# Performance work log

Hardware: AMD Instinct MI355X
Metric: run time of the kernel (lower is better)

Reference implementation:

```python
import jax, jax.numpy as jnp
import numpy as np

TEMPERATURE = 0.5
EPS_NORM = 1e-12   # F.normalize eps
EPS_DEN = 1e-8     # denominator clamp


def setup_inputs() -> dict:
    key = jax.random.key(0)
    k1, k2 = jax.random.split(key)
    B, D = 4096, 256
    return {
        "proj_feat1": jax.random.normal(k1, (B, D), dtype=jnp.float32),
        "proj_feat2": jax.random.normal(k2, (B, D), dtype=jnp.float32),
    }


def _l2_normalize(x):
    n = jnp.sqrt(jnp.sum(x * x, axis=1, keepdims=True))
    return x / jnp.maximum(n, EPS_NORM)


def reference(proj_feat1, proj_feat2):
    B = proj_feat1.shape[0]
    z1 = _l2_normalize(proj_feat1)
    z2 = _l2_normalize(proj_feat2)
    z = jnp.concatenate([z1, z2], axis=0)          # [2B, D], unit rows
    # cosine similarity of unit-norm rows == plain matmul (GEMM instead of
    # the O(N^2*D) broadcasted intermediate in the torch source)
    sim = jnp.matmul(z, z.T)                        # [2B, 2B]
    s = jnp.exp(sim / TEMPERATURE)                  # [2B, 2B]
    idx = jnp.arange(2 * B)
    pos_idx = (idx + B) % (2 * B)                   # roll(eye, B, dim=1) positions
    numerator = s[idx, pos_idx]                     # [2B]
    # negatives: everything except the diagonal
    diag = jnp.diagonal(s)
    denominator = jnp.sum(s, axis=1) - diag         # sum * (1 - eye)
    denominator = jnp.maximum(denominator, EPS_DEN)
    loss = jnp.mean(-jnp.log(numerator / denominator))
    return loss
```

## Files before the change

### kernel.cpp

```cpp
#include <hip/hip_runtime.h>
#include <hip/hip_bf16.h>

#define NTOT 8192
#define BB   4096
#define DD   256

typedef __attribute__((ext_vector_type(8))) short short8v;
typedef __attribute__((ext_vector_type(4))) float f32x4;

__device__ __forceinline__ unsigned short f2bf(float f) {
    union { __hip_bfloat16 h; unsigned short u; } cv;
    cv.h = __float2bfloat16(f);
    return cv.u;
}

__global__ __launch_bounds__(256) void k_normalize(
    const float* __restrict__ x1, const float* __restrict__ x2,
    unsigned short* __restrict__ zbf,
    float* __restrict__ selfdot, float* __restrict__ posdot,
    float* __restrict__ out)
{
    if (blockIdx.x == 0 && threadIdx.x == 0) out[0] = 0.0f;

    const int lane = threadIdx.x & 63;
    const int pair = blockIdx.x * 4 + (threadIdx.x >> 6);

    const float4 a = *(const float4*)(x1 + (size_t)pair * DD + lane * 4);
    const float4 b = *(const float4*)(x2 + (size_t)pair * DD + lane * 4);

    float s1 = a.x * a.x + a.y * a.y + a.z * a.z + a.w * a.w;
    float s2 = b.x * b.x + b.y * b.y + b.z * b.z + b.w * b.w;
#pragma unroll
    for (int off = 1; off < 64; off <<= 1) {
        s1 += __shfl_xor(s1, off);
        s2 += __shfl_xor(s2, off);
    }
    const float inv1 = 1.0f / fmaxf(sqrtf(s1), 1e-12f);
    const float inv2 = 1.0f / fmaxf(sqrtf(s2), 1e-12f);

    const float4 z1 = make_float4(a.x * inv1, a.y * inv1, a.z * inv1, a.w * inv1);
    const float4 z2 = make_float4(b.x * inv2, b.y * inv2, b.z * inv2, b.w * inv2);

    float sd1 = z1.x * z1.x + z1.y * z1.y + z1.z * z1.z + z1.w * z1.w;
    float sd2 = z2.x * z2.x + z2.y * z2.y + z2.z * z2.z + z2.w * z2.w;
    float pd  = z1.x * z2.x + z1.y * z2.y + z1.z * z2.z + z1.w * z2.w;
#pragma unroll
    for (int off = 1; off < 64; off <<= 1) {
        sd1 += __shfl_xor(sd1, off);
        sd2 += __shfl_xor(sd2, off);
        pd  += __shfl_xor(pd, off);
    }

    ushort4 u1, u2;
    u1.x = f2bf(z1.x); u1.y = f2bf(z1.y); u1.z = f2bf(z1.z); u1.w = f2bf(z1.w);
    u2.x = f2bf(z2.x); u2.y = f2bf(z2.y); u2.z = f2bf(z2.z); u2.w = f2bf(z2.w);
    *(ushort4*)(zbf + (size_t)pair * DD + lane * 4) = u1;
    *(ushort4*)(zbf + (size_t)(pair + BB) * DD + lane * 4) = u2;

    if (lane == 0) {
        selfdot[pair] = sd1;
        selfdot[pair + BB] = sd2;
        posdot[pair] = pd;
        posdot[pair + BB] = pd;
    }
}

__global__ __launch_bounds__(256, 2) void k_simsum(
    const unsigned short* __restrict__ zbf, float* __restrict__ S_part)
{
    __shared__ char Bsh[2][32768];

    const int tid  = threadIdx.x;
    const int lane = tid & 63;
    const int wave = tid >> 6;
    const int frow = lane & 15;
    const int row0 = blockIdx.x * 256 + wave * 64;
    const int colStart = blockIdx.y * 512;

    short8v Afrag[4][8];
#pragma unroll
    for (int rt = 0; rt < 4; ++rt) {
        const int row = row0 + rt * 16 + frow;
        const unsigned short* ap = zbf + (size_t)row * DD + (lane >> 4) * 8;
#pragma unroll
        for (int kk = 0; kk < 8; ++kk)
            Afrag[rt][kk] = *(const short8v*)(ap + kk * 32);
    }
#pragma unroll
    for (int rt = 0; rt < 4; ++rt)
#pragma unroll
        for (int kk = 0; kk < 8; ++kk)
            asm volatile("" : "+v"(Afrag[rt][kk]));

    const int jswz = (tid & 31) ^ ((tid >> 5) & 7);
    const char* gsrc0 = (const char*)zbf + (size_t)colStart * 512
                        + (tid >> 5) * 512 + jswz * 16;

    const int base0 = frow * 512 + (lane >> 4) * 16;
    const int bmask = (frow & 7) << 4;

    float rs[4][4];
#pragma unroll
    for (int rt = 0; rt < 4; ++rt)
#pragma unroll
        for (int q = 0; q < 4; ++q) rs[rt][q] = 0.0f;

#pragma unroll
    for (int r = 0; r < 8; ++r)
        __builtin_amdgcn_global_load_lds(
            (const __attribute__((address_space(1))) unsigned int*)(gsrc0 + r * 4096),
            (__attribute__((address_space(3))) unsigned int*)(&Bsh[0][0] + tid * 16 + r * 4096),
            16, 0, 0);
    __syncthreads();

    int cur = 0;
    for (int t = 0; t < 8; ++t) {
        if (t < 7) {
            const char* gs = gsrc0 + (size_t)(t + 1) * 32768;
            char* ld = &Bsh[cur ^ 1][0] + tid * 16;
#pragma unroll
            for (int r = 0; r < 8; ++r)
                __builtin_amdgcn_global_load_lds(
                    (const __attribute__((address_space(1))) unsigned int*)(gs + r * 4096),
                    (__attribute__((address_space(3))) unsigned int*)(ld + r * 4096),
                    16, 0, 0);
        }

#pragma unroll
        for (int c2 = 0; c2 < 2; ++c2) {
            f32x4 acc[4][2];
#pragma unroll
            for (int rt = 0; rt < 4; ++rt)
#pragma unroll
                for (int c = 0; c < 2; ++c) {
                    acc[rt][c][0] = 0.0f; acc[rt][c][1] = 0.0f;
                    acc[rt][c][2] = 0.0f; acc[rt][c][3] = 0.0f;
                }

#pragma unroll
            for (int kk = 0; kk < 8; ++kk) {
                const char* bp = &Bsh[cur][0] + ((base0 + kk * 64) ^ bmask)
                                 + c2 * 16384;
                short8v b0 = *(const short8v*)(bp);
                short8v b1 = *(const short8v*)(bp + 8192);
#pragma unroll
                for (int rt = 0; rt < 4; ++rt) {
                    acc[rt][0] = __builtin_amdgcn_mfma_f32_16x16x32_bf16(
                        Afrag[rt][kk], b0, acc[rt][0], 0, 0, 0);
                    acc[rt][1] = __builtin_amdgcn_mfma_f32_16x16x32_bf16(
                        Afrag[rt][kk], b1, acc[rt][1], 0, 0, 0);
                }
            }

#pragma unroll
            for (int rt = 0; rt < 4; ++rt)
#pragma unroll
                for (int q = 0; q < 4; ++q)
                    rs[rt][q] += exp2f(acc[rt][0][q] * 2.8853900817779268f)
                               + exp2f(acc[rt][1][q] * 2.8853900817779268f);
        }

        __syncthreads();
        cur ^= 1;
    }

#pragma unroll
    for (int rt = 0; rt < 4; ++rt) {
#pragma unroll
        for (int q = 0; q < 4; ++q) {
            float v = rs[rt][q];
            v += __shfl_xor(v, 1);
            v += __shfl_xor(v, 2);
            v += __shfl_xor(v, 4);
            v += __shfl_xor(v, 8);
            if (frow == 0) {
                const int row = row0 + rt * 16 + (lane >> 4) * 4 + q;
                S_part[blockIdx.y * NTOT + row] = v;
            }
        }
    }
}

__global__ __launch_bounds__(256) void k_final(
    const float* __restrict__ S_part, const float* __restrict__ selfdot,
    const float* __restrict__ posdot, float* __restrict__ out)
{
    __shared__ float red[4];
    const int tid = threadIdx.x;
    const int i = blockIdx.x * 256 + tid;
    float s = 0.0f;
#pragma unroll
    for (int sp = 0; sp < 16; ++sp) s += S_part[sp * NTOT + i];
    const float den = fmaxf(s - expf(2.0f * selfdot[i]), 1e-8f);
    float acc = logf(den) - 2.0f * posdot[i];
#pragma unroll
    for (int off = 1; off < 64; off <<= 1) acc += __shfl_xor(acc, off);
    if ((tid & 63) == 0) red[tid >> 6] = acc;
    __syncthreads();
    if (tid == 0)
        atomicAdd(out, (red[0] + red[1] + red[2] + red[3]) * (1.0f / (float)NTOT));
}

extern "C" void kernel_launch(void* const* d_in, const int* in_sizes, int n_in,
                              void* d_out, int out_size, void* d_ws, size_t ws_size,
                              hipStream_t stream) {
    const float* x1 = (const float*)d_in[0];
    const float* x2 = (const float*)d_in[1];
    float* out = (float*)d_out;

    char* ws = (char*)d_ws;
    unsigned short* zbf = (unsigned short*)ws;
    size_t off = (size_t)NTOT * DD * sizeof(unsigned short);
    float* S_part = (float*)(ws + off);
    off += (size_t)16 * NTOT * sizeof(float);
    float* selfdot = (float*)(ws + off);
    off += (size_t)NTOT * sizeof(float);
    float* posdot = (float*)(ws + off);

    k_normalize<<<dim3(BB / 4), dim3(256), 0, stream>>>(x1, x2, zbf, selfdot, posdot, out);
    k_simsum<<<dim3(32, 16), dim3(256), 0, stream>>>(zbf, S_part);
    k_final<<<dim3(32), dim3(256), 0, stream>>>(S_part, selfdot, posdot, out);
}
```

Baseline: 108.2 us.

## Load B fragments directly from global memory, drop LDS double buffering

Replaces the LDS double-buffered staging of B tiles (global_load_lds, swizzling, barriers) with direct per-lane global loads of B fragments in 32-column chunks. Each wave now loads the same B data independently, relying on L1/L2 caching instead of shared memory. This removes barriers and LDS traffic, but it adds redundant global/L1 loads and exposes load latency to the MFMA loop. Grid sizes are now expressed through an NSTRIPE macro.

```diff
diff --git a/kernel.cpp b/kernel.cpp
--- a/kernel.cpp
+++ b/kernel.cpp
@@ -4,6 +4,7 @@
 #define NTOT 8192
 #define BB   4096
 #define DD   256
+#define NSTRIPE 16
 
 typedef __attribute__((ext_vector_type(8))) short short8v;
 typedef __attribute__((ext_vector_type(4))) float f32x4;
@@ -68,36 +69,22 @@
 __global__ __launch_bounds__(256, 2) void k_simsum(
     const unsigned short* __restrict__ zbf, float* __restrict__ S_part)
 {
-    __shared__ char Bsh[2][32768];
-
     const int tid  = threadIdx.x;
     const int lane = tid & 63;
     const int wave = tid >> 6;
     const int frow = lane & 15;
+    const int khalf = (lane >> 4) * 8;
     const int row0 = blockIdx.x * 256 + wave * 64;
     const int colStart = blockIdx.y * 512;
 
     short8v Afrag[4][8];
 #pragma unroll
     for (int rt = 0; rt < 4; ++rt) {
-        const int row = row0 + rt * 16 + frow;
-        const unsigned short* ap = zbf + (size_t)row * DD + (lane >> 4) * 8;
+        const unsigned short* ap = zbf + (size_t)(row0 + rt * 16 + frow) * DD + khalf;
 #pragma unroll
         for (int kk = 0; kk < 8; ++kk)
             Afrag[rt][kk] = *(const short8v*)(ap + kk * 32);
     }
-#pragma unroll
-    for (int rt = 0; rt < 4; ++rt)
-#pragma unroll
-        for (int kk = 0; kk < 8; ++kk)
-            asm volatile("" : "+v"(Afrag[rt][kk]));
-
-    const int jswz = (tid & 31) ^ ((tid >> 5) & 7);
-    const char* gsrc0 = (const char*)zbf + (size_t)colStart * 512
-                        + (tid >> 5) * 512 + jswz * 16;
-
-    const int base0 = frow * 512 + (lane >> 4) * 16;
-    const int bmask = (frow & 7) << 4;
 
     float rs[4][4];
 #pragma unroll
@@ -105,63 +92,39 @@
 #pragma unroll
         for (int q = 0; q < 4; ++q) rs[rt][q] = 0.0f;
 
+#pragma unroll 2
+    for (int ch = 0; ch < 16; ++ch) {
+        const unsigned short* bp = zbf
+            + (size_t)(colStart + ch * 32 + frow) * DD + khalf;
+
+        f32x4 acc[4][2];
 #pragma unroll
-    for (int r = 0; r < 8; ++r)
-        __builtin_amdgcn_global_load_lds(
-            (const __attribute__((address_space(1))) unsigned int*)(gsrc0 + r * 4096),
-            (__attribute__((address_space(3))) unsigned int*)(&Bsh[0][0] + tid * 16 + r * 4096),
-            16, 0, 0);
-    __syncthreads();
+        for (int rt = 0; rt < 4; ++rt)
+#pragma unroll
+            for (int c = 0; c < 2; ++c) {
+                acc[rt][c][0] = 0.0f; acc[rt][c][1] = 0.0f;
+                acc[rt][c][2] = 0.0f; acc[rt][c][3] = 0.0f;
+            }
 
-    int cur = 0;
-    for (int t = 0; t < 8; ++t) {
-        if (t < 7) {
-            const char* gs = gsrc0 + (size_t)(t + 1) * 32768;
-            char* ld = &Bsh[cur ^ 1][0] + tid * 16;
 #pragma unroll
-            for (int r = 0; r < 8; ++r)
-                __builtin_amdgcn_global_load_lds(
-                    (const __attribute__((address_space(1))) unsigned int*)(gs + r * 4096),
-                    (__attribute__((address_space(3))) unsigned int*)(ld + r * 4096),
-                    16, 0, 0);
+        for (int kk = 0; kk < 8; ++kk) {
+            const short8v b0 = *(const short8v*)(bp + kk * 32);
+            const short8v b1 = *(const short8v*)(bp + 16 * DD + kk * 32);
+#pragma unroll
+            for (int rt = 0; rt < 4; ++rt) {
+                acc[rt][0] = __builtin_amdgcn_mfma_f32_16x16x32_bf16(
+                    Afrag[rt][kk], b0, acc[rt][0], 0, 0, 0);
+                acc[rt][1] = __builtin_amdgcn_mfma_f32_16x16x32_bf16(
+                    Afrag[rt][kk], b1, acc[rt][1], 0, 0, 0);
+            }
         }
 
 #pragma unroll
-        for (int c2 = 0; c2 < 2; ++c2) {
-            f32x4 acc[4][2];
+        for (int rt = 0; rt < 4; ++rt)
 #pragma unroll
-            for (int rt = 0; rt < 4; ++rt)
-#pragma unroll
-                for (int c = 0; c < 2; ++c) {
-                    acc[rt][c][0] = 0.0f; acc[rt][c][1] = 0.0f;
-                    acc[rt][c][2] = 0.0f; acc[rt][c][3] = 0.0f;
-                }
-
-#pragma unroll
-            for (int kk = 0; kk < 8; ++kk) {
-                const char* bp = &Bsh[cur][0] + ((base0 + kk * 64) ^ bmask)
-                                 + c2 * 16384;
-                short8v b0 = *(const short8v*)(bp);
-                short8v b1 = *(const short8v*)(bp + 8192);
-#pragma unroll
-                for (int rt = 0; rt < 4; ++rt) {
-                    acc[rt][0] = __builtin_amdgcn_mfma_f32_16x16x32_bf16(
-                        Afrag[rt][kk], b0, acc[rt][0], 0, 0, 0);
-                    acc[rt][1] = __builtin_amdgcn_mfma_f32_16x16x32_bf16(
-                        Afrag[rt][kk], b1, acc[rt][1], 0, 0, 0);
-                }
-            }
-
-#pragma unroll
-            for (int rt = 0; rt < 4; ++rt)
-#pragma unroll
-                for (int q = 0; q < 4; ++q)
-                    rs[rt][q] += exp2f(acc[rt][0][q] * 2.8853900817779268f)
-                               + exp2f(acc[rt][1][q] * 2.8853900817779268f);
-        }
-
-        __syncthreads();
-        cur ^= 1;
+            for (int q = 0; q < 4; ++q)
+                rs[rt][q] += exp2f(acc[rt][0][q] * 2.8853900817779268f)
+                           + exp2f(acc[rt][1][q] * 2.8853900817779268f);
     }
 
 #pragma unroll
@@ -190,7 +153,7 @@
     const int i = blockIdx.x * 256 + tid;
     float s = 0.0f;
 #pragma unroll
-    for (int sp = 0; sp < 16; ++sp) s += S_part[sp * NTOT + i];
+    for (int sp = 0; sp < NSTRIPE; ++sp) s += S_part[sp * NTOT + i];
     const float den = fmaxf(s - expf(2.0f * selfdot[i]), 1e-8f);
     float acc = logf(den) - 2.0f * posdot[i];
 #pragma unroll
@@ -212,12 +175,12 @@
     unsigned short* zbf = (unsigned short*)ws;
     size_t off = (size_t)NTOT * DD * sizeof(unsigned short);
     float* S_part = (float*)(ws + off);
-    off += (size_t)16 * NTOT * sizeof(float);
+    off += (size_t)NSTRIPE * NTOT * sizeof(float);
     float* selfdot = (float*)(ws + off);
     off += (size_t)NTOT * sizeof(float);
     float* posdot = (float*)(ws + off);
 
     k_normalize<<<dim3(BB / 4), dim3(256), 0, stream>>>(x1, x2, zbf, selfdot, posdot, out);
-    k_simsum<<<dim3(32, 16), dim3(256), 0, stream>>>(zbf, S_part);
-    k_final<<<dim3(32), dim3(256), 0, stream>>>(S_part, selfdot, posdot, out);
+    k_simsum<<<dim3(32, NSTRIPE), dim3(256), 0, stream>>>(zbf, S_part);
+    k_final<<<dim3(NTOT / 256), dim3(256), 0, stream>>>(S_part, selfdot, posdot, out);
 }
```

Measured after the change: 139.7 us. 1.29x slower.

## Exploit similarity symmetry with triangular tiling and balanced persistent work split

Applied to the files above, without the earlier changes.

Computes only the upper-triangular blocks of the symmetric similarity matrix. Each tile's exp values are added to the row sums and, for off-diagonal tiles, also to the column sums, through atomics into a single zeroed sum vector. The triangular steps are spread evenly over 512 blocks, so a block can cross row-panel boundaries and reload its A fragments. This roughly halves the MFMA and exp work, in exchange for float atomics (nondeterministic summation order) and extra shuffle reductions.

```diff
diff --git a/kernel.cpp b/kernel.cpp
--- a/kernel.cpp
+++ b/kernel.cpp
@@ -4,6 +4,8 @@
 #define NTOT 8192
 #define BB   4096
 #define DD   256
+#define NBLK 512
+#define NSTEPS 2112
 
 typedef __attribute__((ext_vector_type(8))) short short8v;
 typedef __attribute__((ext_vector_type(4))) float f32x4;
@@ -18,9 +20,13 @@
     const float* __restrict__ x1, const float* __restrict__ x2,
     unsigned short* __restrict__ zbf,
     float* __restrict__ selfdot, float* __restrict__ posdot,
-    float* __restrict__ out)
+    float* __restrict__ S, float* __restrict__ out)
 {
-    if (blockIdx.x == 0 && threadIdx.x == 0) out[0] = 0.0f;
+    if (blockIdx.x < 8) {
+        float4 z4 = make_float4(0.f, 0.f, 0.f, 0.f);
+        *(float4*)(S + blockIdx.x * 1024 + threadIdx.x * 4) = z4;
+        if (blockIdx.x == 0 && threadIdx.x == 0) out[0] = 0.0f;
+    }
 
     const int lane = threadIdx.x & 63;
     const int pair = blockIdx.x * 4 + (threadIdx.x >> 6);
@@ -66,7 +72,7 @@
 }
 
 __global__ __launch_bounds__(256, 2) void k_simsum(
-    const unsigned short* __restrict__ zbf, float* __restrict__ S_part)
+    const unsigned short* __restrict__ zbf, float* __restrict__ S)
 {
     __shared__ char Bsh[2][32768];
 
@@ -74,60 +80,76 @@
     const int lane = tid & 63;
     const int wave = tid >> 6;
     const int frow = lane & 15;
-    const int row0 = blockIdx.x * 256 + wave * 64;
-    const int colStart = blockIdx.y * 512;
+
+    const int b = blockIdx.x;
+    const int sBeg = (33 * b) >> 3;
+    const int sEnd = (33 * (b + 1)) >> 3;
+
+    int ai = 0;
+    {
+        int C = 0;
+        while (C + 128 - 4 * ai <= sBeg) { C += 128 - 4 * ai; ++ai; }
+    }
+    int C2 = 0;
+    for (int k = 0; k < ai; ++k) C2 += 128 - 4 * k;
+    int ct = sBeg - C2;
+
+    const int jswz = (tid & 31) ^ ((tid >> 5) & 7);
+    const int stageOff = (tid >> 5) * 512 + jswz * 16;
+
+    const int base0 = frow * 512 + (lane >> 4) * 16;
+    const int bmask = (frow & 7) << 4;
+    int addrs[8];
+#pragma unroll
+    for (int kk = 0; kk < 8; ++kk) addrs[kk] = (base0 + kk * 64) ^ bmask;
 
     short8v Afrag[4][8];
 #pragma unroll
     for (int rt = 0; rt < 4; ++rt) {
-        const int row = row0 + rt * 16 + frow;
-        const unsigned short* ap = zbf + (size_t)row * DD + (lane >> 4) * 8;
+        const unsigned short* ap =
+            zbf + (size_t)(256 * ai + wave * 64 + rt * 16 + frow) * DD + (lane >> 4) * 8;
 #pragma unroll
         for (int kk = 0; kk < 8; ++kk)
             Afrag[rt][kk] = *(const short8v*)(ap + kk * 32);
     }
+
+    float rs[4][4];
 #pragma unroll
     for (int rt = 0; rt < 4; ++rt)
 #pragma unroll
-        for (int kk = 0; kk < 8; ++kk)
-            asm volatile("" : "+v"(Afrag[rt][kk]));
-
-    const int jswz = (tid & 31) ^ ((tid >> 5) & 7);
-    const char* gsrc0 = (const char*)zbf + (size_t)colStart * 512
-                        + (tid >> 5) * 512 + jswz * 16;
-
-    const int base0 = frow * 512 + (lane >> 4) * 16;
-    const int bmask = (frow & 7) << 4;
-
-    float rs[4][4];
-#pragma unroll
-    for (int rt = 0; rt < 4; ++rt)
-#pragma unroll
         for (int q = 0; q < 4; ++q) rs[rt][q] = 0.0f;
 
-#pragma unroll
-    for (int r = 0; r < 8; ++r)
-        __builtin_amdgcn_global_load_lds(
-            (const __attribute__((address_space(1))) unsigned int*)(gsrc0 + r * 4096),
-            (__attribute__((address_space(3))) unsigned int*)(&Bsh[0][0] + tid * 16 + r * 4096),
-            16, 0, 0);
+#define COLBASE(ii, tt) ((tt) < 4 ? 256 * (ii) + 64 * (tt) : 256 * ((ii) + 1) + 64 * ((tt) - 4))
+
+#define STAGE(cb, bufidx)                                                          \
+    do {                                                                           \
+        const char* gs_ = (const char*)zbf + (size_t)(cb) * 512 + stageOff;        \
+        char* ld_ = &Bsh[bufidx][0] + tid * 16;                                    \
+        _Pragma("unroll")                                                          \
+        for (int r_ = 0; r_ < 8; ++r_)                                             \
+            __builtin_amdgcn_global_load_lds(                                      \
+                (const __attribute__((address_space(1))) unsigned int*)(gs_ + r_ * 4096), \
+                (__attribute__((address_space(3))) unsigned int*)(ld_ + r_ * 4096),\
+                16, 0, 0);                                                         \
+    } while (0)
+
+    STAGE(COLBASE(ai, ct), 0);
     __syncthreads();
 
     int cur = 0;
-    for (int t = 0; t < 8; ++t) {
-        if (t < 7) {
-            const char* gs = gsrc0 + (size_t)(t + 1) * 32768;
-            char* ld = &Bsh[cur ^ 1][0] + tid * 16;
-#pragma unroll
-            for (int r = 0; r < 8; ++r)
-                __builtin_amdgcn_global_load_lds(
-                    (const __attribute__((address_space(1))) unsigned int*)(gs + r * 4096),
-                    (__attribute__((address_space(3))) unsigned int*)(ld + r * 4096),
-                    16, 0, 0);
-        }
+    int ci = ai, cstep = ct;
+    for (int s = sBeg; s < sEnd; ++s) {
+        int ni = ci, nt = cstep + 1;
+        if (nt >= 128 - 4 * ci) { ni = ci + 1; nt = 0; }
+        if (s + 1 < sEnd) STAGE(COLBASE(ni, nt), cur ^ 1);
+
+        const int  colbase = COLBASE(ci, cstep);
+        const bool isUpper = (cstep >= 4);
+        const char* bsh = &Bsh[cur][0];
 
 #pragma unroll
         for (int c2 = 0; c2 < 2; ++c2) {
+            const char* bc = bsh + c2 * 16384;
             f32x4 acc[4][2];
 #pragma unroll
             for (int rt = 0; rt < 4; ++rt)
@@ -139,10 +161,8 @@
 
 #pragma unroll
             for (int kk = 0; kk < 8; ++kk) {
-                const char* bp = &Bsh[cur][0] + ((base0 + kk * 64) ^ bmask)
-                                 + c2 * 16384;
-                short8v b0 = *(const short8v*)(bp);
-                short8v b1 = *(const short8v*)(bp + 8192);
+                const short8v b0 = *(const short8v*)(bc + addrs[kk]);
+                const short8v b1 = *(const short8v*)(bc + addrs[kk] + 8192);
 #pragma unroll
                 for (int rt = 0; rt < 4; ++rt) {
                     acc[rt][0] = __builtin_amdgcn_mfma_f32_16x16x32_bf16(
@@ -152,20 +172,58 @@
                 }
             }
 
+            float cs0 = 0.0f, cs1 = 0.0f;
 #pragma unroll
             for (int rt = 0; rt < 4; ++rt)
 #pragma unroll
-                for (int q = 0; q < 4; ++q)
-                    rs[rt][q] += exp2f(acc[rt][0][q] * 2.8853900817779268f)
-                               + exp2f(acc[rt][1][q] * 2.8853900817779268f);
+                for (int q = 0; q < 4; ++q) {
+                    const float e0 = exp2f(acc[rt][0][q] * 2.8853900817779268f);
+                    const float e1 = exp2f(acc[rt][1][q] * 2.8853900817779268f);
+                    rs[rt][q] += e0 + e1;
+                    cs0 += e0; cs1 += e1;
+                }
+            if (isUpper) {
+                cs0 += __shfl_xor(cs0, 16); cs0 += __shfl_xor(cs0, 32);
+                cs1 += __shfl_xor(cs1, 16); cs1 += __shfl_xor(cs1, 32);
+                if (lane < 16) {
+                    atomicAdd(&S[colbase + c2 * 32 + frow], cs0);
+                    atomicAdd(&S[colbase + c2 * 32 + 16 + frow], cs1);
+                }
+            }
         }
+
+        if (s + 1 < sEnd && ni != ai) {
+#pragma unroll
+            for (int rt = 0; rt < 4; ++rt)
+#pragma unroll
+                for (int q = 0; q < 4; ++q) {
+                    float v = rs[rt][q];
+                    v += __shfl_xor(v, 1);
+                    v += __shfl_xor(v, 2);
+                    v += __shfl_xor(v, 4);
+                    v += __shfl_xor(v, 8);
+                    if (frow == 0)
+                        atomicAdd(&S[256 * ai + wave * 64 + rt * 16 + (lane >> 4) * 4 + q], v);
+                    rs[rt][q] = 0.0f;
+                }
+            ai = ni;
+#pragma unroll
+            for (int rt = 0; rt < 4; ++rt) {
+                const unsigned short* ap =
+                    zbf + (size_t)(256 * ai + wave * 64 + rt * 16 + frow) * DD + (lane >> 4) * 8;
+#pragma unroll
+                for (int kk = 0; kk < 8; ++kk)
+                    Afrag[rt][kk] = *(const short8v*)(ap + kk * 32);
+            }
+        }
+        ci = ni; cstep = nt;
 
         __syncthreads();
         cur ^= 1;
     }
 
 #pragma unroll
-    for (int rt = 0; rt < 4; ++rt) {
+    for (int rt = 0; rt < 4; ++rt)
 #pragma unroll
         for (int q = 0; q < 4; ++q) {
             float v = rs[rt][q];
@@ -173,25 +231,21 @@
             v += __shfl_xor(v, 2);
             v += __shfl_xor(v, 4);
             v += __shfl_xor(v, 8);
-            if (frow == 0) {
-                const int row = row0 + rt * 16 + (lane >> 4) * 4 + q;
-                S_part[blockIdx.y * NTOT + row] = v;
-            }
+            if (frow == 0)
+                atomicAdd(&S[256 * ai + wave * 64 + rt * 16 + (lane >> 4) * 4 + q], v);
         }
-    }
+#undef STAGE
+#undef COLBASE
 }
 
 __global__ __launch_bounds__(256) void k_final(
-    const float* __restrict__ S_part, const float* __restrict__ selfdot,
+    const float* __restrict__ S, const float* __restrict__ selfdot,
     const float* __restrict__ posdot, float* __restrict__ out)
 {
     __shared__ float red[4];
     const int tid = threadIdx.x;
     const int i = blockIdx.x * 256 + tid;
-    float s = 0.0f;
-#pragma unroll
-    for (int sp = 0; sp < 16; ++sp) s += S_part[sp * NTOT + i];
-    const float den = fmaxf(s - expf(2.0f * selfdot[i]), 1e-8f);
+    const float den = fmaxf(S[i] - expf(2.0f * selfdot[i]), 1e-8f);
     float acc = logf(den) - 2.0f * posdot[i];
 #pragma unroll
     for (int off = 1; off < 64; off <<= 1) acc += __shfl_xor(acc, off);
@@ -211,13 +265,13 @@
     char* ws = (char*)d_ws;
     unsigned short* zbf = (unsigned short*)ws;
     size_t off = (size_t)NTOT * DD * sizeof(unsigned short);
-    float* S_part = (float*)(ws + off);
-    off += (size_t)16 * NTOT * sizeof(float);
+    float* S = (float*)(ws + off);
+    off += (size_t)NTOT * sizeof(float);
     float* selfdot = (float*)(ws + off);
     off += (size_t)NTOT * sizeof(float);
     float* posdot = (float*)(ws + off);
 
-    k_normalize<<<dim3(BB / 4), dim3(256), 0, stream>>>(x1, x2, zbf, selfdot, posdot, out);
-    k_simsum<<<dim3(32, 16), dim3(256), 0, stream>>>(zbf, S_part);
-    k_final<<<dim3(32), dim3(256), 0, stream>>>(S_part, selfdot, posdot, out);
-}
+    k_normalize<<<dim3(BB / 4), dim3(256), 0, stream>>>(x1, x2, zbf, selfdot, posdot, S, out);
+    k_simsum<<<dim3(NBLK), dim3(256), 0, stream>>>(zbf, S);
+    k_final<<<dim3(NTOT / 256), dim3(256), 0, stream>>>(S, selfdot, posdot, out);
+}
```

Measured after the change: 100.6 us. 1.08x faster.
